# Kernel tuning notes

Measured on AMD Instinct MI355X. Metric: run time of the kernel, lower is better.

Reference implementation:

```python
import math
import jax, jax.numpy as jnp
import numpy as np

N_NODES = 100000
N_EDGES = 3200000
D = 128
H = 8
DK = D // H


def setup_inputs() -> dict:
    key = jax.random.key(0)
    ks = jax.random.split(key, 12)
    s = 1.0 / math.sqrt(D)
    return {
        "feat": jax.random.normal(ks[0], (N_NODES, D), jnp.float32),
        "Wk": jax.random.normal(ks[1], (D, D), jnp.float32) * s,
        "bk": jax.random.normal(ks[2], (D,), jnp.float32) * s,
        "Wq": jax.random.normal(ks[3], (D, D), jnp.float32) * s,
        "bq": jax.random.normal(ks[4], (D,), jnp.float32) * s,
        "Wv": jax.random.normal(ks[5], (D, D), jnp.float32) * s,
        "bv": jax.random.normal(ks[6], (D,), jnp.float32) * s,
        "w_att": jax.random.normal(ks[7], (H, DK, DK), jnp.float32) * (1.0 / math.sqrt(DK)),
        "w_msg": jax.random.normal(ks[8], (H, DK, DK), jnp.float32) * (1.0 / math.sqrt(DK)),
        "mu": jax.random.uniform(ks[9], (1,), jnp.float32, 0.5, 1.5),
        "src": jax.random.randint(ks[10], (N_EDGES,), 0, N_NODES, jnp.int32),
        "dst": jax.random.randint(ks[11], (N_EDGES,), 0, N_NODES, jnp.int32),
    }


def reference(feat, Wk, bk, Wq, bq, Wv, bv, w_att, w_msg, mu, src, dst):
    N = feat.shape[0]
    # node projections, per-head relation transforms
    k = (feat @ Wk.T + bk).reshape(N, H, DK)            # (N,H,dk)
    v = (feat @ Wv.T + bv).reshape(N, H, DK)
    q = (feat @ Wq.T + bq).reshape(N, H, DK)
    k = jnp.einsum('nhi,hij->nhj', k, w_att)
    v = jnp.einsum('nhi,hij->nhj', v, w_msg)
    # edge-wise q (dst) . k (src) attention logits
    logits = jnp.einsum('ehd,ehd->eh', q[dst], k[src])  # (E,H)
    logits = logits * (mu[0] / math.sqrt(DK))
    # segment softmax over incoming edges of each dst node
    m = jax.ops.segment_max(logits, dst, num_segments=N)   # (N,H)
    ex = jnp.exp(logits - m[dst])
    denom = jax.ops.segment_sum(ex, dst, num_segments=N)   # (N,H)
    attn = ex / denom[dst]                                  # (E,H)
    # weighted message aggregation
    msg = v[src] * attn[..., None]                          # (E,H,dk)
    h = jax.ops.segment_sum(msg, dst, num_segments=N)       # (N,H,dk)
    return h.reshape(N, H * DK)
```

## Files before the change

### kernel.cpp

```cpp
#include <hip/hip_runtime.h>
#include <hip/hip_bf16.h>
#include <stdint.h>

#define DD 128
#define HH 8
#define DKK 16

#define BSHIFT 7
#define BNODES (1 << BSHIFT)
#define SC_EPT 16

typedef __attribute__((ext_vector_type(8))) short bf16x8;
typedef __attribute__((ext_vector_type(4))) float f32x4;

__device__ __forceinline__ float bfhi2f(unsigned u) {
  union { unsigned i; float f; } c; c.i = u & 0xFFFF0000u; return c.f;
}
__device__ __forceinline__ float bflo2f(unsigned u) {
  union { unsigned i; float f; } c; c.i = u << 16; return c.f;
}
__device__ __forceinline__ unsigned short f2bf(float f) {
  __hip_bfloat16 b = __float2bfloat16(f);
  return *reinterpret_cast<unsigned short*>(&b);
}

__global__ __launch_bounds__(256) void prep_weights(
    const float* __restrict__ Wq, const float* __restrict__ bq,
    const float* __restrict__ Wk, const float* __restrict__ bk,
    const float* __restrict__ Wv, const float* __restrict__ bv,
    const float* __restrict__ w_att, const float* __restrict__ w_msg,
    const float* __restrict__ mu,
    unsigned short* __restrict__ WcatT, float* __restrict__ bcat) {
  int gid = blockIdx.x * blockDim.x + threadIdx.x;
  if (gid >= DD * 384) return;
  int f = gid / 384;
  int o = gid % 384;
  float scale = mu[0] * 0.25f;
  float w;
  if (o < 128) {
    w = Wq[o * DD + f] * scale;
  } else if (o < 256) {
    int c = o - 128, h = c >> 4, j = c & 15;
    float s = 0.f;
#pragma unroll
    for (int i = 0; i < 16; ++i)
      s += Wk[(h * 16 + i) * DD + f] * w_att[h * 256 + i * 16 + j];
    w = s;
  } else {
    int c = o - 256, h = c >> 4, j = c & 15;
    float s = 0.f;
#pragma unroll
    for (int i = 0; i < 16; ++i)
      s += Wv[(h * 16 + i) * DD + f] * w_msg[h * 256 + i * 16 + j];
    w = s;
  }
  WcatT[(size_t)o * DD + f] = f2bf(w);
  if (f == 0) {
    float b;
    if (o < 128) {
      b = bq[o] * scale;
    } else if (o < 256) {
      int c = o - 128, h = c >> 4, j = c & 15;
      float s = 0.f;
#pragma unroll
      for (int i = 0; i < 16; ++i)
        s += bk[h * 16 + i] * w_att[h * 256 + i * 16 + j];
      b = s;
    } else {
      int c = o - 256, h = c >> 4, j = c & 15;
      float s = 0.f;
#pragma unroll
      for (int i = 0; i < 16; ++i)
        s += bv[h * 16 + i] * w_msg[h * 256 + i * 16 + j];
      b = s;
    }
    bcat[o] = b;
  }
}

__global__ __launch_bounds__(256) void proj_gemm(
    const float* __restrict__ feat, const unsigned short* __restrict__ WcatT,
    const float* __restrict__ bcat, float* __restrict__ Q,
    __hip_bfloat16* __restrict__ Vb, unsigned char* __restrict__ KVrow,
    int N) {
  int row0 = blockIdx.x * 64;
  int wave = threadIdx.x >> 6, lane = threadIdx.x & 63;
  int lrow = lane & 15, lk = lane >> 4;
  int arow = row0 + wave * 16 + lrow;
  const float* ap = feat + (size_t)(arow < N ? arow : 0) * DD;

  bf16x8 a[4];
#pragma unroll
  for (int ks = 0; ks < 4; ++ks) {
    float4 a0 = *(const float4*)(ap + ks * 32 + lk * 8);
    float4 a1 = *(const float4*)(ap + ks * 32 + lk * 8 + 4);
    union { bf16x8 v; unsigned short s[8]; } u;
    u.s[0] = f2bf(a0.x); u.s[1] = f2bf(a0.y);
    u.s[2] = f2bf(a0.z); u.s[3] = f2bf(a0.w);
    u.s[4] = f2bf(a1.x); u.s[5] = f2bf(a1.y);
    u.s[6] = f2bf(a1.z); u.s[7] = f2bf(a1.w);
    a[ks] = u.v;
  }

  int outrow = row0 + wave * 16 + lk * 4;
#pragma unroll
  for (int nf = 0; nf < 24; ++nf) {
    f32x4 acc = (f32x4){0.f, 0.f, 0.f, 0.f};
#pragma unroll
    for (int ks = 0; ks < 4; ++ks) {
      bf16x8 b = *(const bf16x8*)(WcatT + (size_t)(nf * 16 + lrow) * DD +
                                  ks * 32 + lk * 8);
      acc = __builtin_amdgcn_mfma_f32_16x16x32_bf16(a[ks], b, acc, 0, 0, 0);
    }
    int col = nf * 16 + lrow;
    float bias = bcat[col];
#pragma unroll
    for (int r = 0; r < 4; ++r) {
      int grow = outrow + r;
      if (grow >= N) continue;
      float c = acc[r] + bias;
      if (col < 128) {
        Q[(size_t)grow * DD + col] = c;
      } else if (col < 256) {
        int cc = col - 128, h = cc >> 4, d = cc & 15;
        *(__hip_bfloat16*)(KVrow + (size_t)grow * 384 + h * 48 + d * 2) =
            __float2bfloat16(c);
      } else {
        Vb[(size_t)grow * DD + (col - 256)] = __float2bfloat16(c);
      }
    }
  }
}

__global__ __launch_bounds__(256) void quantize_v(
    const __hip_bfloat16* __restrict__ Vb, unsigned char* __restrict__ KVrow,
    unsigned short* __restrict__ S, int NH) {
  int g = blockIdx.x * 256 + threadIdx.x;
  if (g >= NH) return;
  const unsigned* vp = (const unsigned*)Vb + (size_t)g * 8;
  float v[16];
#pragma unroll
  for (int w = 0; w < 8; ++w) {
    unsigned u = vp[w];
    v[w * 2] = bflo2f(u); v[w * 2 + 1] = bfhi2f(u);
  }
  float mv = 0.f;
#pragma unroll
  for (int j = 0; j < 16; ++j) mv = fmaxf(mv, fabsf(v[j]));
  float iv = (mv > 0.f) ? 127.f / mv : 0.f;
  unsigned outw[4];
#pragma unroll
  for (int w = 0; w < 4; ++w) {
    unsigned pv = 0;
#pragma unroll
    for (int b = 0; b < 4; ++b) {
      int qv = (int)rintf(v[w * 4 + b] * iv) + 128;
      qv = qv < 0 ? 0 : (qv > 255 ? 255 : qv);
      pv |= (unsigned)qv << (8 * b);
    }
    outw[w] = pv;
  }
  int node = g >> 3, h = g & 7;
  *(uint4*)(KVrow + (size_t)node * 384 + h * 48 + 32) =
      make_uint4(outw[0], outw[1], outw[2], outw[3]);
  S[g] = f2bf(mv / 127.f);
}

__global__ __launch_bounds__(256) void bucket_hist(
    const int* __restrict__ dst, int* __restrict__ bucket_count, int E,
    int NB) {
  __shared__ int h[1024];
  int tid = threadIdx.x;
  for (int i = tid; i < NB; i += 256) h[i] = 0;
  __syncthreads();
  for (int e = blockIdx.x * blockDim.x + tid; e < E;
       e += gridDim.x * blockDim.x)
    atomicAdd(&h[dst[e] >> BSHIFT], 1);
  __syncthreads();
  for (int i = tid; i < NB; i += 256)
    if (h[i]) atomicAdd(&bucket_count[i], h[i]);
}

__global__ __launch_bounds__(64) void bucket_scan(
    const int* __restrict__ bucket_count, int* __restrict__ bucket_base,
    int* __restrict__ bucket_cursor, int NB) {
  int lane = threadIdx.x;
  int running = 0;
  for (int c0 = 0; c0 < NB; c0 += 64) {
    int idx = c0 + lane;
    int v = (idx < NB) ? bucket_count[idx] : 0;
    int s = v;
#pragma unroll
    for (int off = 1; off < 64; off <<= 1) {
      int t = __shfl_up(s, off);
      if (lane >= off) s += t;
    }
    int excl = running + s - v;
    if (idx < NB) {
      bucket_base[idx] = excl;
      bucket_cursor[idx] = excl;
    }
    running += __shfl(s, 63);
  }
}

__global__ __launch_bounds__(256) void bucket_scatter(
    const int* __restrict__ src, const int* __restrict__ dst,
    int* __restrict__ bucket_cursor, unsigned* __restrict__ ebuf, int E,
    int NB) {
  __shared__ int h[1024];
  __shared__ int cur[1024];
  int tid = threadIdx.x;
  int base0 = blockIdx.x * (256 * SC_EPT);
  for (int i = tid; i < NB; i += 256) h[i] = 0;
  __syncthreads();
  int myd[SC_EPT], mys[SC_EPT];
#pragma unroll
  for (int i = 0; i < SC_EPT; ++i) {
    int e = base0 + i * 256 + tid;
    if (e < E) {
      myd[i] = dst[e];
      mys[i] = src[e];
      atomicAdd(&h[myd[i] >> BSHIFT], 1);
    } else {
      myd[i] = -1;
    }
  }
  __syncthreads();
  for (int i = tid; i < NB; i += 256)
    cur[i] = h[i] ? atomicAdd(&bucket_cursor[i], h[i]) : 0;
  __syncthreads();
#pragma unroll
  for (int i = 0; i < SC_EPT; ++i) {
    if (myd[i] >= 0) {
      int b = myd[i] >> BSHIFT;
      int p = atomicAdd(&cur[b], 1);
      ebuf[p] = ((unsigned)(myd[i] & (BNODES - 1)) << 17) | (unsigned)mys[i];
    }
  }
}

__global__ __launch_bounds__(256) void bucket_to_csr(
    const unsigned* __restrict__ ebuf, const int* __restrict__ bucket_base,
    const int* __restrict__ bucket_count, int* __restrict__ rowptr,
    int* __restrict__ deg, int* __restrict__ esrc, int N) {
  __shared__ int h[BNODES];
  __shared__ int sc[BNODES];
  __shared__ int cur[BNODES];
  int b = blockIdx.x;
  int tid = threadIdx.x;
  int start = bucket_base[b];
  int cnt = bucket_count[b];
  if (tid < BNODES) h[tid] = 0;
  __syncthreads();
  for (int i = tid; i < cnt; i += 256)
    atomicAdd(&h[ebuf[start + i] >> 17], 1);
  __syncthreads();
  if (tid < BNODES) sc[tid] = h[tid];
  __syncthreads();
  for (int off = 1; off < BNODES; off <<= 1) {
    int t = 0;
    if (tid < BNODES && tid >= off) t = sc[tid - off];
    __syncthreads();
    if (tid < BNODES) sc[tid] += t;
    __syncthreads();
  }
  if (tid < BNODES) {
    int excl = sc[tid] - h[tid];
    int node = b * BNODES + tid;
    if (node < N) {
      rowptr[node] = start + excl;
      deg[node] = h[tid];
    }
    cur[tid] = excl;
  }
  __syncthreads();
  for (int i = tid; i < cnt; i += 256) {
    unsigned u = ebuf[start + i];
    int p = atomicAdd(&cur[u >> 17], 1);
    esrc[start + p] = (int)(u & 0x1FFFFu);
  }
}

__global__ __launch_bounds__(256) void node_aggregate(
    const int* __restrict__ esrc, const int* __restrict__ rowptr,
    const int* __restrict__ deg, const float* __restrict__ Q,
    const unsigned char* __restrict__ KVrow,
    const unsigned short* __restrict__ S,
    float* __restrict__ out, int N) {
  int n = blockIdx.x * 4 + (threadIdx.x >> 6);
  if (n >= N) return;
  int lane = threadIdx.x & 63;
  int h = lane & 7;
  int p = lane >> 3;

  float q[16];
#pragma unroll
  for (int i = 0; i < 4; ++i) {
    float4 t = *(const float4*)(Q + (size_t)n * DD + h * DKK + i * 4);
    q[i * 4 + 0] = t.x; q[i * 4 + 1] = t.y;
    q[i * 4 + 2] = t.z; q[i * 4 + 3] = t.w;
  }
  int row = rowptr[n];
  int dg = deg[n];

  float acc[16];
#pragma unroll
  for (int j = 0; j < 16; ++j) acc[j] = 0.f;
  float den = 0.f, evsum = 0.f;

  for (int base = 0; base < dg; base += 64) {
    int myid = (base + lane < dg) ? esrc[row + base + lane] : 0;
    int cnt = min(64, dg - base);
    int iters = (cnt + 7) >> 3;
#pragma unroll 2
    for (int i = 0; i < iters; ++i) {
      int slot = i * 8 + p;
      int s = __shfl(myid, slot);
      float m = (base + slot < dg) ? 1.f : 0.f;
      const unsigned char* rp = KVrow + (size_t)s * 384 + h * 48;
      uint4 k0 = *(const uint4*)rp;
      uint4 k1 = *(const uint4*)(rp + 16);
      uint4 vq = *(const uint4*)(rp + 32);
      float sV = bflo2f((unsigned)S[(size_t)s * 8 + h]);
      float dot;
      dot = q[0] * bflo2f(k0.x);
      dot = fmaf(q[1], bfhi2f(k0.x), dot);
      dot = fmaf(q[2], bflo2f(k0.y), dot);
      dot = fmaf(q[3], bfhi2f(k0.y), dot);
      dot = fmaf(q[4], bflo2f(k0.z), dot);
      dot = fmaf(q[5], bfhi2f(k0.z), dot);
      dot = fmaf(q[6], bflo2f(k0.w), dot);
      dot = fmaf(q[7], bfhi2f(k0.w), dot);
      dot = fmaf(q[8], bflo2f(k1.x), dot);
      dot = fmaf(q[9], bfhi2f(k1.x), dot);
      dot = fmaf(q[10], bflo2f(k1.y), dot);
      dot = fmaf(q[11], bfhi2f(k1.y), dot);
      dot = fmaf(q[12], bflo2f(k1.z), dot);
      dot = fmaf(q[13], bfhi2f(k1.z), dot);
      dot = fmaf(q[14], bflo2f(k1.w), dot);
      dot = fmaf(q[15], bfhi2f(k1.w), dot);
      float ex = m * __expf(fminf(dot, 80.f));
      den += ex;
      float evs = ex * sV;
      evsum += evs;
      acc[0] = fmaf(evs, (float)(vq.x & 255), acc[0]);
      acc[1] = fmaf(evs, (float)((vq.x >> 8) & 255), acc[1]);
      acc[2] = fmaf(evs, (float)((vq.x >> 16) & 255), acc[2]);
      acc[3] = fmaf(evs, (float)(vq.x >> 24), acc[3]);
      acc[4] = fmaf(evs, (float)(vq.y & 255), acc[4]);
      acc[5] = fmaf(evs, (float)((vq.y >> 8) & 255), acc[5]);
      acc[6] = fmaf(evs, (float)((vq.y >> 16) & 255), acc[6]);
      acc[7] = fmaf(evs, (float)(vq.y >> 24), acc[7]);
      acc[8] = fmaf(evs, (float)(vq.z & 255), acc[8]);
      acc[9] = fmaf(evs, (float)((vq.z >> 8) & 255), acc[9]);
      acc[10] = fmaf(evs, (float)((vq.z >> 16) & 255), acc[10]);
      acc[11] = fmaf(evs, (float)(vq.z >> 24), acc[11]);
      acc[12] = fmaf(evs, (float)(vq.w & 255), acc[12]);
      acc[13] = fmaf(evs, (float)((vq.w >> 8) & 255), acc[13]);
      acc[14] = fmaf(evs, (float)((vq.w >> 16) & 255), acc[14]);
      acc[15] = fmaf(evs, (float)(vq.w >> 24), acc[15]);
    }
  }

#pragma unroll
  for (int j = 0; j < 16; ++j) {
    acc[j] += __shfl_xor(acc[j], 8);
    acc[j] += __shfl_xor(acc[j], 16);
    acc[j] += __shfl_xor(acc[j], 32);
  }
  den += __shfl_xor(den, 8);
  den += __shfl_xor(den, 16);
  den += __shfl_xor(den, 32);
  evsum += __shfl_xor(evsum, 8);
  evsum += __shfl_xor(evsum, 16);
  evsum += __shfl_xor(evsum, 32);

  if (p == 0) {
    float inv = (dg > 0 && den > 0.f) ? 1.0f / den : 0.f;
    float corr = 128.f * evsum;
#pragma unroll
    for (int i = 0; i < 4; ++i) {
      float4 o = make_float4((acc[i * 4 + 0] - corr) * inv,
                             (acc[i * 4 + 1] - corr) * inv,
                             (acc[i * 4 + 2] - corr) * inv,
                             (acc[i * 4 + 3] - corr) * inv);
      *(float4*)(out + (size_t)n * DD + h * DKK + i * 4) = o;
    }
  }
}

extern "C" void kernel_launch(void* const* d_in, const int* in_sizes, int n_in,
                              void* d_out, int out_size, void* d_ws,
                              size_t ws_size, hipStream_t stream) {
  const float* feat = (const float*)d_in[0];
  const float* Wk = (const float*)d_in[1];
  const float* bk = (const float*)d_in[2];
  const float* Wq = (const float*)d_in[3];
  const float* bq = (const float*)d_in[4];
  const float* Wv = (const float*)d_in[5];
  const float* bv = (const float*)d_in[6];
  const float* w_att = (const float*)d_in[7];
  const float* w_msg = (const float*)d_in[8];
  const float* mu = (const float*)d_in[9];
  const int* src = (const int*)d_in[10];
  const int* dst = (const int*)d_in[11];

  int N = in_sizes[0] / DD;
  int E = in_sizes[10];
  int NB = (N + BNODES - 1) >> BSHIFT;

  char* ws = (char*)d_ws;
  unsigned short* WcatT = (unsigned short*)ws; ws += (size_t)DD * 384 * 2;
  float* bcat = (float*)ws; ws += 384 * 4;
  ws = (char*)(((uintptr_t)ws + 255) & ~(uintptr_t)255);
  float* Q = (float*)ws; ws += (size_t)N * DD * 4;
  __hip_bfloat16* Vb = (__hip_bfloat16*)ws; ws += (size_t)N * DD * 2;
  unsigned char* KVrow = (unsigned char*)ws; ws += (size_t)N * 384;
  ws = (char*)(((uintptr_t)ws + 255) & ~(uintptr_t)255);
  unsigned short* S = (unsigned short*)ws; ws += (size_t)N * HH * 2;
  ws = (char*)(((uintptr_t)ws + 255) & ~(uintptr_t)255);
  int* deg = (int*)ws; ws += (size_t)N * 4;
  int* rowptr = (int*)ws; ws += (size_t)N * 4;
  int* bucket_count = (int*)ws; ws += 1024 * 4;
  int* bucket_base = (int*)ws; ws += 1024 * 4;
  int* bucket_cursor = (int*)ws; ws += 1024 * 4;
  ws = (char*)(((uintptr_t)ws + 255) & ~(uintptr_t)255);
  unsigned* ebuf = (unsigned*)ws; ws += (size_t)E * 4;
  int* esrc = (int*)ws; ws += (size_t)E * 4;

  hipMemsetAsync(bucket_count, 0, 1024 * 4, stream);

  prep_weights<<<(DD * 384 + 255) / 256, 256, 0, stream>>>(
      Wq, bq, Wk, bk, Wv, bv, w_att, w_msg, mu, WcatT, bcat);

  proj_gemm<<<(N + 63) / 64, 256, 0, stream>>>(feat, WcatT, bcat, Q, Vb,
                                               KVrow, N);

  quantize_v<<<(N * HH + 255) / 256, 256, 0, stream>>>(Vb, KVrow, S, N * HH);

  bucket_hist<<<256, 256, 0, stream>>>(dst, bucket_count, E, NB);
  bucket_scan<<<1, 64, 0, stream>>>(bucket_count, bucket_base, bucket_cursor,
                                    NB);
  int sc_blocks = (E + 256 * SC_EPT - 1) / (256 * SC_EPT);
  bucket_scatter<<<sc_blocks, 256, 0, stream>>>(src, dst, bucket_cursor, ebuf,
                                                E, NB);
  bucket_to_csr<<<NB, 256, 0, stream>>>(ebuf, bucket_base, bucket_count,
                                        rowptr, deg, esrc, N);

  node_aggregate<<<(N + 3) / 4, 256, 0, stream>>>(esrc, rowptr, deg, Q, KVrow,
                                                  S, (float*)d_out, N);
}
```

Measured before the change: 414.6 us.

## Fuse V quantization into projection GEMM and use fp16 dot2 for attention logits

New measurement: 387.6 us. 6.5% less time.

```diff
diff --git a/kernel.cpp b/kernel.cpp
--- a/kernel.cpp
+++ b/kernel.cpp
@@ -1,5 +1,6 @@
 #include <hip/hip_runtime.h>
 #include <hip/hip_bf16.h>
+#include <hip/hip_fp16.h>
 #include <stdint.h>
 
 #define DD 128
@@ -12,6 +13,8 @@
 
 typedef __attribute__((ext_vector_type(8))) short bf16x8;
 typedef __attribute__((ext_vector_type(4))) float f32x4;
+typedef _Float16 h2 __attribute__((ext_vector_type(2)));
+union u32h2 { unsigned u; h2 h; };
 
 __device__ __forceinline__ float bfhi2f(unsigned u) {
   union { unsigned i; float f; } c; c.i = u & 0xFFFF0000u; return c.f;
@@ -81,89 +84,80 @@
 __global__ __launch_bounds__(256) void proj_gemm(
     const float* __restrict__ feat, const unsigned short* __restrict__ WcatT,
     const float* __restrict__ bcat, float* __restrict__ Q,
-    __hip_bfloat16* __restrict__ Vb, unsigned char* __restrict__ KVrow,
+    unsigned char* __restrict__ KVrow, unsigned short* __restrict__ S,
     int N) {
-  int row0 = blockIdx.x * 64;
+  int row0 = blockIdx.x * 128;
   int wave = threadIdx.x >> 6, lane = threadIdx.x & 63;
   int lrow = lane & 15, lk = lane >> 4;
-  int arow = row0 + wave * 16 + lrow;
-  const float* ap = feat + (size_t)(arow < N ? arow : 0) * DD;
-
-  bf16x8 a[4];
-#pragma unroll
-  for (int ks = 0; ks < 4; ++ks) {
-    float4 a0 = *(const float4*)(ap + ks * 32 + lk * 8);
-    float4 a1 = *(const float4*)(ap + ks * 32 + lk * 8 + 4);
-    union { bf16x8 v; unsigned short s[8]; } u;
-    u.s[0] = f2bf(a0.x); u.s[1] = f2bf(a0.y);
-    u.s[2] = f2bf(a0.z); u.s[3] = f2bf(a0.w);
-    u.s[4] = f2bf(a1.x); u.s[5] = f2bf(a1.y);
-    u.s[6] = f2bf(a1.z); u.s[7] = f2bf(a1.w);
-    a[ks] = u.v;
-  }
-
-  int outrow = row0 + wave * 16 + lk * 4;
+
+  bf16x8 a0[4], a1[4];
+#pragma unroll
+  for (int fr = 0; fr < 2; ++fr) {
+    int arow = row0 + wave * 32 + fr * 16 + lrow;
+    const float* ap = feat + (size_t)(arow < N ? arow : 0) * DD;
+#pragma unroll
+    for (int ks = 0; ks < 4; ++ks) {
+      float4 v0 = *(const float4*)(ap + ks * 32 + lk * 8);
+      float4 v1 = *(const float4*)(ap + ks * 32 + lk * 8 + 4);
+      union { bf16x8 v; unsigned short s[8]; } u;
+      u.s[0] = f2bf(v0.x); u.s[1] = f2bf(v0.y);
+      u.s[2] = f2bf(v0.z); u.s[3] = f2bf(v0.w);
+      u.s[4] = f2bf(v1.x); u.s[5] = f2bf(v1.y);
+      u.s[6] = f2bf(v1.z); u.s[7] = f2bf(v1.w);
+      if (fr == 0) a0[ks] = u.v; else a1[ks] = u.v;
+    }
+  }
+
 #pragma unroll
   for (int nf = 0; nf < 24; ++nf) {
-    f32x4 acc = (f32x4){0.f, 0.f, 0.f, 0.f};
+    f32x4 acc0 = (f32x4){0.f, 0.f, 0.f, 0.f};
+    f32x4 acc1 = (f32x4){0.f, 0.f, 0.f, 0.f};
 #pragma unroll
     for (int ks = 0; ks < 4; ++ks) {
       bf16x8 b = *(const bf16x8*)(WcatT + (size_t)(nf * 16 + lrow) * DD +
                                   ks * 32 + lk * 8);
-      acc = __builtin_amdgcn_mfma_f32_16x16x32_bf16(a[ks], b, acc, 0, 0, 0);
+      acc0 = __builtin_amdgcn_mfma_f32_16x16x32_bf16(a0[ks], b, acc0, 0, 0, 0);
+      acc1 = __builtin_amdgcn_mfma_f32_16x16x32_bf16(a1[ks], b, acc1, 0, 0, 0);
     }
     int col = nf * 16 + lrow;
     float bias = bcat[col];
 #pragma unroll
-    for (int r = 0; r < 4; ++r) {
-      int grow = outrow + r;
-      if (grow >= N) continue;
-      float c = acc[r] + bias;
-      if (col < 128) {
-        Q[(size_t)grow * DD + col] = c;
-      } else if (col < 256) {
-        int cc = col - 128, h = cc >> 4, d = cc & 15;
-        *(__hip_bfloat16*)(KVrow + (size_t)grow * 384 + h * 48 + d * 2) =
-            __float2bfloat16(c);
-      } else {
-        Vb[(size_t)grow * DD + (col - 256)] = __float2bfloat16(c);
+    for (int fr = 0; fr < 2; ++fr) {
+      f32x4 acc = fr == 0 ? acc0 : acc1;
+      int outrow = row0 + wave * 32 + fr * 16 + lk * 4;
+#pragma unroll
+      for (int r = 0; r < 4; ++r) {
+        int grow = outrow + r;
+        float c = acc[r] + bias;
+        if (nf < 8) {
+          if (grow < N) Q[(size_t)grow * DD + col] = c;
+        } else if (nf < 16) {
+          int h = nf - 8;
+          if (grow < N)
+            *(__half*)(KVrow + (size_t)grow * 384 + h * 48 + lrow * 2) =
+                __float2half(c);
+        } else {
+          int h = nf - 16;
+          float av = fabsf(c);
+          av = fmaxf(av, __shfl_xor(av, 1));
+          av = fmaxf(av, __shfl_xor(av, 2));
+          av = fmaxf(av, __shfl_xor(av, 4));
+          av = fmaxf(av, __shfl_xor(av, 8));
+          float iv = (av > 0.f) ? 127.f / av : 0.f;
+          int qv = (int)rintf(c * iv) + 128;
+          qv = qv < 0 ? 0 : (qv > 255 ? 255 : qv);
+          unsigned tmp = (unsigned)qv << ((lrow & 3) * 8);
+          tmp |= __shfl_xor(tmp, 1);
+          tmp |= __shfl_xor(tmp, 2);
+          if ((lrow & 3) == 0 && grow < N)
+            *(unsigned*)(KVrow + (size_t)grow * 384 + h * 48 + 32 +
+                         (lrow >> 2) * 4) = tmp;
+          if (lrow == 0 && grow < N)
+            S[(size_t)grow * 8 + h] = f2bf(av / 127.f);
+        }
       }
     }
   }
-}
-
-__global__ __launch_bounds__(256) void quantize_v(
-    const __hip_bfloat16* __restrict__ Vb, unsigned char* __restrict__ KVrow,
-    unsigned short* __restrict__ S, int NH) {
-  int g = blockIdx.x * 256 + threadIdx.x;
-  if (g >= NH) return;
-  const unsigned* vp = (const unsigned*)Vb + (size_t)g * 8;
-  float v[16];
-#pragma unroll
-  for (int w = 0; w < 8; ++w) {
-    unsigned u = vp[w];
-    v[w * 2] = bflo2f(u); v[w * 2 + 1] = bfhi2f(u);
-  }
-  float mv = 0.f;
-#pragma unroll
-  for (int j = 0; j < 16; ++j) mv = fmaxf(mv, fabsf(v[j]));
-  float iv = (mv > 0.f) ? 127.f / mv : 0.f;
-  unsigned outw[4];
-#pragma unroll
-  for (int w = 0; w < 4; ++w) {
-    unsigned pv = 0;
-#pragma unroll
-    for (int b = 0; b < 4; ++b) {
-      int qv = (int)rintf(v[w * 4 + b] * iv) + 128;
-      qv = qv < 0 ? 0 : (qv > 255 ? 255 : qv);
-      pv |= (unsigned)qv << (8 * b);
-    }
-    outw[w] = pv;
-  }
-  int node = g >> 3, h = g & 7;
-  *(uint4*)(KVrow + (size_t)node * 384 + h * 48 + 32) =
-      make_uint4(outw[0], outw[1], outw[2], outw[3]);
-  S[g] = f2bf(mv / 127.f);
 }
 
 __global__ __launch_bounds__(256) void bucket_hist(
@@ -294,12 +288,12 @@
   int h = lane & 7;
   int p = lane >> 3;
 
-  float q[16];
+  h2 qh[8];
 #pragma unroll
   for (int i = 0; i < 4; ++i) {
     float4 t = *(const float4*)(Q + (size_t)n * DD + h * DKK + i * 4);
-    q[i * 4 + 0] = t.x; q[i * 4 + 1] = t.y;
-    q[i * 4 + 2] = t.z; q[i * 4 + 3] = t.w;
+    qh[i * 2 + 0] = (h2){(_Float16)t.x, (_Float16)t.y};
+    qh[i * 2 + 1] = (h2){(_Float16)t.z, (_Float16)t.w};
   }
   int row = rowptr[n];
   int dg = deg[n];
@@ -323,23 +317,18 @@
       uint4 k1 = *(const uint4*)(rp + 16);
       uint4 vq = *(const uint4*)(rp + 32);
       float sV = bflo2f((unsigned)S[(size_t)s * 8 + h]);
-      float dot;
-      dot = q[0] * bflo2f(k0.x);
-      dot = fmaf(q[1], bfhi2f(k0.x), dot);
-      dot = fmaf(q[2], bflo2f(k0.y), dot);
-      dot = fmaf(q[3], bfhi2f(k0.y), dot);
-      dot = fmaf(q[4], bflo2f(k0.z), dot);
-      dot = fmaf(q[5], bfhi2f(k0.z), dot);
-      dot = fmaf(q[6], bflo2f(k0.w), dot);
-      dot = fmaf(q[7], bfhi2f(k0.w), dot);
-      dot = fmaf(q[8], bflo2f(k1.x), dot);
-      dot = fmaf(q[9], bfhi2f(k1.x), dot);
-      dot = fmaf(q[10], bflo2f(k1.y), dot);
-      dot = fmaf(q[11], bfhi2f(k1.y), dot);
-      dot = fmaf(q[12], bflo2f(k1.z), dot);
-      dot = fmaf(q[13], bfhi2f(k1.z), dot);
-      dot = fmaf(q[14], bflo2f(k1.w), dot);
-      dot = fmaf(q[15], bfhi2f(k1.w), dot);
+      u32h2 c0, c1, c2, c3;
+      c0.u = k0.x; c1.u = k0.y; c2.u = k0.z; c3.u = k0.w;
+      float dA = __builtin_amdgcn_fdot2(qh[0], c0.h, 0.f, false);
+      float dB = __builtin_amdgcn_fdot2(qh[1], c1.h, 0.f, false);
+      dA = __builtin_amdgcn_fdot2(qh[2], c2.h, dA, false);
+      dB = __builtin_amdgcn_fdot2(qh[3], c3.h, dB, false);
+      c0.u = k1.x; c1.u = k1.y; c2.u = k1.z; c3.u = k1.w;
+      dA = __builtin_amdgcn_fdot2(qh[4], c0.h, dA, false);
+      dB = __builtin_amdgcn_fdot2(qh[5], c1.h, dB, false);
+      dA = __builtin_amdgcn_fdot2(qh[6], c2.h, dA, false);
+      dB = __builtin_amdgcn_fdot2(qh[7], c3.h, dB, false);
+      float dot = dA + dB;
       float ex = m * __expf(fminf(dot, 80.f));
       den += ex;
       float evs = ex * sV;
@@ -415,7 +404,6 @@
   float* bcat = (float*)ws; ws += 384 * 4;
   ws = (char*)(((uintptr_t)ws + 255) & ~(uintptr_t)255);
   float* Q = (float*)ws; ws += (size_t)N * DD * 4;
-  __hip_bfloat16* Vb = (__hip_bfloat16*)ws; ws += (size_t)N * DD * 2;
   unsigned char* KVrow = (unsigned char*)ws; ws += (size_t)N * 384;
   ws = (char*)(((uintptr_t)ws + 255) & ~(uintptr_t)255);
   unsigned short* S = (unsigned short*)ws; ws += (size_t)N * HH * 2;
@@ -434,10 +422,8 @@
   prep_weights<<<(DD * 384 + 255) / 256, 256, 0, stream>>>(
       Wq, bq, Wk, bk, Wv, bv, w_att, w_msg, mu, WcatT, bcat);
 
-  proj_gemm<<<(N + 63) / 64, 256, 0, stream>>>(feat, WcatT, bcat, Q, Vb,
-                                               KVrow, N);
-
-  quantize_v<<<(N * HH + 255) / 256, 256, 0, stream>>>(Vb, KVrow, S, N * HH);
+  proj_gemm<<<(N + 127) / 128, 256, 0, stream>>>(feat, WcatT, bcat, Q, KVrow,
+                                                 S, N);
 
   bucket_hist<<<256, 256, 0, stream>>>(dst, bucket_count, E, NB);
   bucket_scan<<<1, 64, 0, stream>>>(bucket_count, bucket_base, bucket_cursor,
```
